# Kernel tuning notes

Measured on AMD Instinct MI355X. Metric: run time of the kernel, lower is better.

## Reference

```python
import jax, jax.numpy as jnp
import numpy as np

H = 8      # heads
S = 64     # size per head
EPS = 1e-5

def _ln(x, g, b):
    # LayerNorm over last axis with scale+offset (haiku hk.LayerNorm([-1], True, True))
    m = jnp.mean(x, axis=-1, keepdims=True)
    v = jnp.mean(jnp.square(x - m), axis=-1, keepdims=True)
    return (x - m) * jax.lax.rsqrt(v + EPS) * g + b

def setup_inputs() -> dict:
    key = jax.random.key(0)
    ks = jax.random.split(key, 10)
    N, C, K, CP = 16384, 512, 32, 128
    local = jax.random.normal(ks[0], (N, C), dtype=jnp.float32)
    pair = jax.random.normal(ks[1], (N, K, CP), dtype=jnp.float32)
    neighbours = jax.random.randint(ks[2], (N, K), 0, N, dtype=jnp.int64)
    mask = jnp.ones((N, K), dtype=bool)
    # parameters
    w_qkv = jax.random.normal(ks[3], (C, H * 3 * S), dtype=jnp.float32) / np.sqrt(C)
    g_q = jnp.ones((S,), jnp.float32); b_q = jnp.zeros((S,), jnp.float32)
    g_k = jnp.ones((S,), jnp.float32); b_k = jnp.zeros((S,), jnp.float32)
    w_bias = jax.random.normal(ks[4], (CP, H), dtype=jnp.float32) / np.sqrt(CP)
    d_cat = H * CP + H * S
    w_out = jax.random.normal(ks[5], (d_cat, C), dtype=jnp.float32) / np.sqrt(d_cat)
    b_out = jnp.zeros((C,), jnp.float32)
    return {"local": local, "pair": pair, "neighbours": neighbours, "mask": mask,
            "w_qkv": w_qkv, "g_q": g_q, "b_q": b_q, "g_k": g_k, "b_k": b_k,
            "w_bias": w_bias, "w_out": w_out, "b_out": b_out}

def reference(local, pair, neighbours, mask, w_qkv, g_q, b_q, g_k, b_k, w_bias, w_out, b_out):
    N = local.shape[0]
    qkv = (local @ w_qkv).reshape(N, H, 3 * S)          # [N, H, 3S]
    q, k, v = jnp.split(qkv, 3, axis=-1)                # each [N, H, S]
    q = _ln(q, g_q, b_q)
    k = _ln(k, g_k, b_k)
    bias = jnp.einsum('ijc,ch->ijh', pair, w_bias)      # [N, K, H]
    k_n = k[neighbours]                                 # [N, K, H, S]
    v_n = v[neighbours]                                 # [N, K, H, S]
    dot = jnp.einsum('ihc,ijhc->ijh', q, k_n) * (1.0 / np.sqrt(S))
    w_L = np.sqrt(0.5).astype(np.float32)
    logits = w_L * (dot + bias)                         # [N, K, H]
    pair_mask = mask & (neighbours != -1)               # [N, K]
    logits = jnp.where(pair_mask[..., None], logits, -1e9)
    attn = jax.nn.softmax(logits, axis=-2)              # softmax over neighbours K
    attn = jnp.where(pair_mask[..., None], attn, 0.0)
    out_pair = jnp.einsum('ijh,ijc->ihc', attn, pair)   # [N, H, CP]
    out_scalar = jnp.einsum('ijh,ijhc->ihc', attn, v_n) # [N, H, S]
    cat = jnp.concatenate((out_pair.reshape(N, -1), out_scalar.reshape(N, -1)), axis=-1)
    out = cat @ w_out + b_out                           # [N, C]
    return out.astype(local.dtype)
```

## Files before the change

kernel.cpp:

```cpp
#include <hip/hip_runtime.h>
#include <hip/hip_bf16.h>
#include <cstdint>

#define NTOK 16384
#define CDIM 512
#define KNB 32
#define CPD 128
#define NH 8
#define SD 64
#define QKV_W 1536
#define DCAT 1536

typedef __attribute__((ext_vector_type(8))) short short8;
typedef __attribute__((ext_vector_type(4))) float f32x4;

__device__ inline float bl16(unsigned w) { return __uint_as_float(w << 16); }
__device__ inline float bh16(unsigned w) { return __uint_as_float(w & 0xffff0000u); }

__device__ inline ushort bf2u(float x) {
    __hip_bfloat16 b = __float2bfloat16(x);
    return *(const ushort*)&b;
}

__device__ inline void gload_lds16(const void* g, void* l) {
    __builtin_amdgcn_global_load_lds((const __attribute__((address_space(1))) void*)g,
                                     (__attribute__((address_space(3))) void*)l, 16, 0, 0);
}

__global__ __launch_bounds__(256) void cvt_bf16_kernel(const float4* __restrict__ in,
                                                       ushort4* __restrict__ out, int n4)
{
    const int idx = blockIdx.x * 256 + threadIdx.x;
    if (idx < n4) {
        const float4 v = in[idx];
        ushort4 o;
        o.x = bf2u(v.x); o.y = bf2u(v.y); o.z = bf2u(v.z); o.w = bf2u(v.w);
        out[idx] = o;
    }
}

__global__ __launch_bounds__(256) void transpose_cvt(const float* __restrict__ in,
                                                     __hip_bfloat16* __restrict__ out,
                                                     int R, int Cc)
{
    __shared__ float t[32][33];
    const int c0 = blockIdx.x * 32, r0 = blockIdx.y * 32;
    const int tx = threadIdx.x & 31, ty = threadIdx.x >> 5;
    #pragma unroll
    for (int rr = ty; rr < 32; rr += 8)
        t[rr][tx] = in[(size_t)(r0 + rr) * Cc + c0 + tx];
    __syncthreads();
    #pragma unroll
    for (int rr = ty; rr < 32; rr += 8)
        out[(size_t)(c0 + rr) * R + r0 + tx] = __float2bfloat16(t[tx][rr]);
}

template<bool ADD_BIAS>
__global__ __launch_bounds__(256) void gemm_bf16(const ushort* __restrict__ A,
                                                 const ushort* __restrict__ Bt,
                                                 const float* __restrict__ bias,
                                                 float* __restrict__ C,
                                                 int M, int N, int K)
{
    __shared__ __align__(16) ushort Asl[128 * 32];
    __shared__ __align__(16) ushort Bsl[128 * 32];

    const int tid = threadIdx.x;
    const int wave = tid >> 6;
    const int lane = tid & 63;
    const int m0 = blockIdx.y * 128;
    const int n0 = blockIdx.x * 128;
    const int wr = wave >> 1, wc = wave & 1;

    f32x4 acc[4][4] = {};

    const int st_row_in_chunk = lane >> 2;
    const int st_bcol = (lane & 3) * 16;

    const int lr = lane & 15;
    const int kg = lane >> 4;

    for (int kt = 0; kt < K; kt += 32) {
        #pragma unroll
        for (int p = 0; p < 2; ++p) {
            const int chunk = wave * 2 + p;
            const int row = chunk * 16 + st_row_in_chunk;
            const char* asrc = (const char*)(A + (size_t)(m0 + row) * K + kt) + st_bcol;
            const char* bsrc = (const char*)(Bt + (size_t)(n0 + row) * K + kt) + st_bcol;
            gload_lds16(asrc, (char*)Asl + chunk * 1024);
            gload_lds16(bsrc, (char*)Bsl + chunk * 1024);
        }
        __syncthreads();

        short8 a[4], b[4];
        #pragma unroll
        for (int m = 0; m < 4; ++m)
            a[m] = *(const short8*)&Asl[(wr * 64 + m * 16 + lr) * 32 + kg * 8];
        #pragma unroll
        for (int n = 0; n < 4; ++n)
            b[n] = *(const short8*)&Bsl[(wc * 64 + n * 16 + lr) * 32 + kg * 8];
        #pragma unroll
        for (int m = 0; m < 4; ++m)
            #pragma unroll
            for (int n = 0; n < 4; ++n)
                acc[m][n] = __builtin_amdgcn_mfma_f32_16x16x32_bf16(a[m], b[n], acc[m][n], 0, 0, 0);
        __syncthreads();
    }

    #pragma unroll
    for (int m = 0; m < 4; ++m) {
        #pragma unroll
        for (int n = 0; n < 4; ++n) {
            const int col = n0 + wc * 64 + n * 16 + lr;
            const float bv = ADD_BIAS ? bias[col] : 0.0f;
            #pragma unroll
            for (int r = 0; r < 4; ++r) {
                const int row = m0 + wr * 64 + m * 16 + kg * 4 + r;
                C[(size_t)row * N + col] = acc[m][n][r] + bv;
            }
        }
    }
}

__global__ __launch_bounds__(256) void ln_kernel(const float* __restrict__ qkv,
                                                 const float* __restrict__ g_q,
                                                 const float* __restrict__ b_q,
                                                 const float* __restrict__ g_k,
                                                 const float* __restrict__ b_k,
                                                 __hip_bfloat16* __restrict__ qc,
                                                 __hip_bfloat16* __restrict__ kc,
                                                 __hip_bfloat16* __restrict__ vc)
{
    const int gid = blockIdx.x * 4 + (threadIdx.x >> 6);
    const int lane = threadIdx.x & 63;

    const float* p = qkv + (size_t)(gid >> 3) * QKV_W + (gid & 7) * 192;
    const float q = p[lane];
    const float k = p[64 + lane];
    const float v = p[128 + lane];

    float sq = q, sk = k;
    #pragma unroll
    for (int o = 1; o < 64; o <<= 1) { sq += __shfl_xor(sq, o); sk += __shfl_xor(sk, o); }
    const float mq = sq * (1.0f / 64.0f), mk = sk * (1.0f / 64.0f);
    const float dq = q - mq, dk = k - mk;
    float vq = dq * dq, vk = dk * dk;
    #pragma unroll
    for (int o = 1; o < 64; o <<= 1) { vq += __shfl_xor(vq, o); vk += __shfl_xor(vk, o); }
    const float iq = rsqrtf(vq * (1.0f / 64.0f) + 1e-5f);
    const float ik = rsqrtf(vk * (1.0f / 64.0f) + 1e-5f);

    const size_t o64 = (size_t)gid * 64 + lane;
    qc[o64] = __float2bfloat16(dq * iq * g_q[lane] + b_q[lane]);
    kc[o64] = __float2bfloat16(dk * ik * g_k[lane] + b_k[lane]);
    vc[o64] = __float2bfloat16(v);
}

__global__ __launch_bounds__(256) void attn_kernel(const __hip_bfloat16* __restrict__ qc,
                                                   const __hip_bfloat16* __restrict__ kc,
                                                   const __hip_bfloat16* __restrict__ vc,
                                                   const float* __restrict__ pair,
                                                   const int* __restrict__ nbr,
                                                   const float* __restrict__ w_bias,
                                                   __hip_bfloat16* __restrict__ cat)
{
    __shared__ __align__(16) ushort s_pairb[KNB][CPD + 8];
    __shared__ __align__(16) ushort s_wbTb[NH][CPD + 8];
    __shared__ __align__(16) ushort s_qb[NH][SD + 8];
    __shared__ __align__(16) float s_att[NH][KNB + 4];
    __shared__ __align__(16) float s_att2[NH][KNB + 4];
    __shared__ int s_nb[KNB];

    const int i = blockIdx.x;
    const int tid = threadIdx.x;
    const int j = tid >> 3;
    const int h = tid & 7;
    const int wave = tid >> 6;
    const int lane = tid & 63;

    const int rowj = nbr[i * KNB + j];
    const int rk = rowj < 0 ? 0 : rowj;
    const uint4* kp = (const uint4*)(kc + ((size_t)rk * NH + h) * SD);
    uint4 ka0 = kp[0], ka1 = kp[1], ka2 = kp[2], ka3 = kp[3];

    if (tid < KNB) s_nb[tid] = nbr[i * KNB + tid];
    if (tid < 64) {
        const uint4 qw = ((const uint4*)(qc + (size_t)i * 512))[tid];
        *(uint4*)&s_qb[tid >> 3][(tid & 7) * 8] = qw;
    }
    {
        const float4 w4 = ((const float4*)w_bias)[tid];
        const int c = tid >> 1;
        const int h0 = (tid & 1) * 4;
        s_wbTb[h0 + 0][c] = bf2u(w4.x);
        s_wbTb[h0 + 1][c] = bf2u(w4.y);
        s_wbTb[h0 + 2][c] = bf2u(w4.z);
        s_wbTb[h0 + 3][c] = bf2u(w4.w);
    }
    {
        const float4* pr = (const float4*)(pair + (size_t)i * KNB * CPD);
        #pragma unroll
        for (int t2 = 0; t2 < 2; ++t2) {
            const int ch = t2 * 256 + tid;
            const int row = ch >> 4;
            const int c8 = (ch & 15) * 8;
            const float4 a = pr[row * 32 + (c8 >> 2)];
            const float4 b = pr[row * 32 + (c8 >> 2) + 1];
            short8 o;
            o[0] = (short)bf2u(a.x); o[1] = (short)bf2u(a.y);
            o[2] = (short)bf2u(a.z); o[3] = (short)bf2u(a.w);
            o[4] = (short)bf2u(b.x); o[5] = (short)bf2u(b.y);
            o[6] = (short)bf2u(b.z); o[7] = (short)bf2u(b.w);
            *(short8*)&s_pairb[row][c8] = o;
        }
    }
    __syncthreads();

    uint4 kb0 = kp[4], kb1 = kp[5], kb2 = kp[6], kb3 = kp[7];

    const uint4* qrow = (const uint4*)&s_qb[h][0];
    float d0 = 0.f, d1 = 0.f, d2 = 0.f, d3 = 0.f;
    #pragma unroll
    for (int u = 0; u < 4; ++u) {
        uint4 K;
        switch (u) { case 0: K = ka0; break; case 1: K = ka1; break;
                     case 2: K = ka2; break; default: K = ka3; break; }
        const uint4 Q = qrow[u];
        d0 = fmaf(bl16(K.x), bl16(Q.x), fmaf(bh16(K.x), bh16(Q.x), d0));
        d1 = fmaf(bl16(K.y), bl16(Q.y), fmaf(bh16(K.y), bh16(Q.y), d1));
        d2 = fmaf(bl16(K.z), bl16(Q.z), fmaf(bh16(K.z), bh16(Q.z), d2));
        d3 = fmaf(bl16(K.w), bl16(Q.w), fmaf(bh16(K.w), bh16(Q.w), d3));
    }

    if (wave < 2) {
        const int lr = lane & 15;
        const int kg = lane >> 4;
        f32x4 cacc = {};
        const ushort* arow = &s_pairb[wave * 16 + lr][kg * 8];
        const ushort* brow = &s_wbTb[lr & 7][kg * 8];
        #pragma unroll
        for (int ks = 0; ks < 4; ++ks) {
            const short8 af = *(const short8*)(arow + ks * 32);
            const short8 bf = *(const short8*)(brow + ks * 32);
            cacc = __builtin_amdgcn_mfma_f32_16x16x32_bf16(af, bf, cacc, 0, 0, 0);
        }
        if (lr < 8) {
            const int jj = wave * 16 + kg * 4;
            s_att[lr][jj + 0] = cacc[0];
            s_att[lr][jj + 1] = cacc[1];
            s_att[lr][jj + 2] = cacc[2];
            s_att[lr][jj + 3] = cacc[3];
        }
    }

    #pragma unroll
    for (int u = 0; u < 4; ++u) {
        uint4 K;
        switch (u) { case 0: K = kb0; break; case 1: K = kb1; break;
                     case 2: K = kb2; break; default: K = kb3; break; }
        const uint4 Q = qrow[u + 4];
        d0 = fmaf(bl16(K.x), bl16(Q.x), fmaf(bh16(K.x), bh16(Q.x), d0));
        d1 = fmaf(bl16(K.y), bl16(Q.y), fmaf(bh16(K.y), bh16(Q.y), d1));
        d2 = fmaf(bl16(K.z), bl16(Q.z), fmaf(bh16(K.z), bh16(Q.z), d2));
        d3 = fmaf(bl16(K.w), bl16(Q.w), fmaf(bh16(K.w), bh16(Q.w), d3));
    }
    __syncthreads();

    float logit = -1e9f;
    if (rowj >= 0) {
        const float dot = (d0 + d1) + (d2 + d3);
        logit = 0.70710678118f * (dot * 0.125f + s_att[h][j]);
    }
    s_att[h][j] = logit;
    __syncthreads();

    const int slot = wave * 16 + (lane & 15);
    const int jg = lane >> 4;
    const int hh = slot >> 3;
    const char* vbase = (const char*)vc;
    uint4 va0, va1, va2, va3;
    {
        const int r0 = s_nb[jg * 8 + 0] < 0 ? 0 : s_nb[jg * 8 + 0];
        const int r1 = s_nb[jg * 8 + 1] < 0 ? 0 : s_nb[jg * 8 + 1];
        const int r2 = s_nb[jg * 8 + 2] < 0 ? 0 : s_nb[jg * 8 + 2];
        const int r3 = s_nb[jg * 8 + 3] < 0 ? 0 : s_nb[jg * 8 + 3];
        va0 = *(const uint4*)(vbase + (size_t)r0 * 1024 + slot * 16);
        va1 = *(const uint4*)(vbase + (size_t)r1 * 1024 + slot * 16);
        va2 = *(const uint4*)(vbase + (size_t)r2 * 1024 + slot * 16);
        va3 = *(const uint4*)(vbase + (size_t)r3 * 1024 + slot * 16);
    }

    {
        float mx = -1e30f;
        #pragma unroll
        for (int t = 0; t < 8; ++t) {
            const float4 w = *(const float4*)&s_att[h][t * 4];
            mx = fmaxf(mx, fmaxf(fmaxf(w.x, w.y), fmaxf(w.z, w.w)));
        }
        float s0 = 0.f, s1 = 0.f;
        #pragma unroll
        for (int t = 0; t < 8; ++t) {
            const float4 w = *(const float4*)&s_att[h][t * 4];
            s0 += __expf(w.x - mx) + __expf(w.z - mx);
            s1 += __expf(w.y - mx) + __expf(w.w - mx);
        }
        float aval = __expf(logit - mx) / (s0 + s1);
        if (rowj < 0) aval = 0.0f;
        s_att2[h][j] = aval;
    }
    __syncthreads();

    const float4 w0 = *(const float4*)&s_att2[hh][jg * 8];
    const float4 w1 = *(const float4*)&s_att2[hh][jg * 8 + 4];

    float acc0 = 0.f, acc1 = 0.f, acc2 = 0.f, acc3 = 0.f;
    float acc4 = 0.f, acc5 = 0.f, acc6 = 0.f, acc7 = 0.f;
    {
        const float a0 = w0.x, a1 = w0.y, a2 = w0.z, a3 = w0.w;
        acc0 = fmaf(a0, bl16(va0.x), acc0); acc1 = fmaf(a0, bh16(va0.x), acc1);
        acc2 = fmaf(a0, bl16(va0.y), acc2); acc3 = fmaf(a0, bh16(va0.y), acc3);
        acc4 = fmaf(a0, bl16(va0.z), acc4); acc5 = fmaf(a0, bh16(va0.z), acc5);
        acc6 = fmaf(a0, bl16(va0.w), acc6); acc7 = fmaf(a0, bh16(va0.w), acc7);
        acc0 = fmaf(a1, bl16(va1.x), acc0); acc1 = fmaf(a1, bh16(va1.x), acc1);
        acc2 = fmaf(a1, bl16(va1.y), acc2); acc3 = fmaf(a1, bh16(va1.y), acc3);
        acc4 = fmaf(a1, bl16(va1.z), acc4); acc5 = fmaf(a1, bh16(va1.z), acc5);
        acc6 = fmaf(a1, bl16(va1.w), acc6); acc7 = fmaf(a1, bh16(va1.w), acc7);
        acc0 = fmaf(a2, bl16(va2.x), acc0); acc1 = fmaf(a2, bh16(va2.x), acc1);
        acc2 = fmaf(a2, bl16(va2.y), acc2); acc3 = fmaf(a2, bh16(va2.y), acc3);
        acc4 = fmaf(a2, bl16(va2.z), acc4); acc5 = fmaf(a2, bh16(va2.z), acc5);
        acc6 = fmaf(a2, bl16(va2.w), acc6); acc7 = fmaf(a2, bh16(va2.w), acc7);
        acc0 = fmaf(a3, bl16(va3.x), acc0); acc1 = fmaf(a3, bh16(va3.x), acc1);
        acc2 = fmaf(a3, bl16(va3.y), acc2); acc3 = fmaf(a3, bh16(va3.y), acc3);
        acc4 = fmaf(a3, bl16(va3.z), acc4); acc5 = fmaf(a3, bh16(va3.z), acc5);
        acc6 = fmaf(a3, bl16(va3.w), acc6); acc7 = fmaf(a3, bh16(va3.w), acc7);
    }
    asm volatile("" ::: "memory");
    uint4 vb0, vb1, vb2, vb3;
    {
        const int r4 = s_nb[jg * 8 + 4] < 0 ? 0 : s_nb[jg * 8 + 4];
        const int r5 = s_nb[jg * 8 + 5] < 0 ? 0 : s_nb[jg * 8 + 5];
        const int r6 = s_nb[jg * 8 + 6] < 0 ? 0 : s_nb[jg * 8 + 6];
        const int r7 = s_nb[jg * 8 + 7] < 0 ? 0 : s_nb[jg * 8 + 7];
        vb0 = *(const uint4*)(vbase + (size_t)r4 * 1024 + slot * 16);
        vb1 = *(const uint4*)(vbase + (size_t)r5 * 1024 + slot * 16);
        vb2 = *(const uint4*)(vbase + (size_t)r6 * 1024 + slot * 16);
        vb3 = *(const uint4*)(vbase + (size_t)r7 * 1024 + slot * 16);
    }
    asm volatile("" ::: "memory");

    {
        const int h2 = tid >> 5;
        const int c0 = (tid & 31) * 4;
        float4 aA = make_float4(0.f, 0.f, 0.f, 0.f);
        float4 aB = make_float4(0.f, 0.f, 0.f, 0.f);
        #pragma unroll
        for (int t = 0; t < 8; ++t) {
            const float4 aw = *(const float4*)&s_att2[h2][t * 4];
            const uint2 p0 = *(const uint2*)&s_pairb[t * 4 + 0][c0];
            const uint2 p1 = *(const uint2*)&s_pairb[t * 4 + 1][c0];
            const uint2 p2 = *(const uint2*)&s_pairb[t * 4 + 2][c0];
            const uint2 p3 = *(const uint2*)&s_pairb[t * 4 + 3][c0];
            aA.x = fmaf(aw.x, bl16(p0.x), aA.x); aA.y = fmaf(aw.x, bh16(p0.x), aA.y);
            aA.z = fmaf(aw.x, bl16(p0.y), aA.z); aA.w = fmaf(aw.x, bh16(p0.y), aA.w);
            aB.x = fmaf(aw.y, bl16(p1.x), aB.x); aB.y = fmaf(aw.y, bh16(p1.x), aB.y);
            aB.z = fmaf(aw.y, bl16(p1.y), aB.z); aB.w = fmaf(aw.y, bh16(p1.y), aB.w);
            aA.x = fmaf(aw.z, bl16(p2.x), aA.x); aA.y = fmaf(aw.z, bh16(p2.x), aA.y);
            aA.z = fmaf(aw.z, bl16(p2.y), aA.z); aA.w = fmaf(aw.z, bh16(p2.y), aA.w);
            aB.x = fmaf(aw.w, bl16(p3.x), aB.x); aB.y = fmaf(aw.w, bh16(p3.x), aB.y);
            aB.z = fmaf(aw.w, bl16(p3.y), aB.z); aB.w = fmaf(aw.w, bh16(p3.y), aB.w);
        }
        ushort4 o;
        o.x = bf2u(aA.x + aB.x); o.y = bf2u(aA.y + aB.y);
        o.z = bf2u(aA.z + aB.z); o.w = bf2u(aA.w + aB.w);
        *(ushort4*)&cat[(size_t)i * DCAT + h2 * CPD + c0] = o;
    }

    {
        const float a4 = w1.x, a5 = w1.y, a6 = w1.z, a7 = w1.w;
        acc0 = fmaf(a4, bl16(vb0.x), acc0); acc1 = fmaf(a4, bh16(vb0.x), acc1);
        acc2 = fmaf(a4, bl16(vb0.y), acc2); acc3 = fmaf(a4, bh16(vb0.y), acc3);
        acc4 = fmaf(a4, bl16(vb0.z), acc4); acc5 = fmaf(a4, bh16(vb0.z), acc5);
        acc6 = fmaf(a4, bl16(vb0.w), acc6); acc7 = fmaf(a4, bh16(vb0.w), acc7);
        acc0 = fmaf(a5, bl16(vb1.x), acc0); acc1 = fmaf(a5, bh16(vb1.x), acc1);
        acc2 = fmaf(a5, bl16(vb1.y), acc2); acc3 = fmaf(a5, bh16(vb1.y), acc3);
        acc4 = fmaf(a5, bl16(vb1.z), acc4); acc5 = fmaf(a5, bh16(vb1.z), acc5);
        acc6 = fmaf(a5, bl16(vb1.w), acc6); acc7 = fmaf(a5, bh16(vb1.w), acc7);
        acc0 = fmaf(a6, bl16(vb2.x), acc0); acc1 = fmaf(a6, bh16(vb2.x), acc1);
        acc2 = fmaf(a6, bl16(vb2.y), acc2); acc3 = fmaf(a6, bh16(vb2.y), acc3);
        acc4 = fmaf(a6, bl16(vb2.z), acc4); acc5 = fmaf(a6, bh16(vb2.z), acc5);
        acc6 = fmaf(a6, bl16(vb2.w), acc6); acc7 = fmaf(a6, bh16(vb2.w), acc7);
        acc0 = fmaf(a7, bl16(vb3.x), acc0); acc1 = fmaf(a7, bh16(vb3.x), acc1);
        acc2 = fmaf(a7, bl16(vb3.y), acc2); acc3 = fmaf(a7, bh16(vb3.y), acc3);
        acc4 = fmaf(a7, bl16(vb3.z), acc4); acc5 = fmaf(a7, bh16(vb3.z), acc5);
        acc6 = fmaf(a7, bl16(vb3.w), acc6); acc7 = fmaf(a7, bh16(vb3.w), acc7);
    }
    acc0 += __shfl_xor(acc0, 16); acc0 += __shfl_xor(acc0, 32);
    acc1 += __shfl_xor(acc1, 16); acc1 += __shfl_xor(acc1, 32);
    acc2 += __shfl_xor(acc2, 16); acc2 += __shfl_xor(acc2, 32);
    acc3 += __shfl_xor(acc3, 16); acc3 += __shfl_xor(acc3, 32);
    acc4 += __shfl_xor(acc4, 16); acc4 += __shfl_xor(acc4, 32);
    acc5 += __shfl_xor(acc5, 16); acc5 += __shfl_xor(acc5, 32);
    acc6 += __shfl_xor(acc6, 16); acc6 += __shfl_xor(acc6, 32);
    acc7 += __shfl_xor(acc7, 16); acc7 += __shfl_xor(acc7, 32);
    if (jg == 0) {
        short8 o;
        o[0] = (short)bf2u(acc0); o[1] = (short)bf2u(acc1);
        o[2] = (short)bf2u(acc2); o[3] = (short)bf2u(acc3);
        o[4] = (short)bf2u(acc4); o[5] = (short)bf2u(acc5);
        o[6] = (short)bf2u(acc6); o[7] = (short)bf2u(acc7);
        char* dst = (char*)cat + ((size_t)i * DCAT + NH * CPD) * 2 + slot * 16;
        *(short8*)dst = o;
    }
}

extern "C" void kernel_launch(void* const* d_in, const int* in_sizes, int n_in,
                              void* d_out, int out_size, void* d_ws, size_t ws_size,
                              hipStream_t stream)
{
    const float* local  = (const float*)d_in[0];
    const float* pair   = (const float*)d_in[1];
    const int*   nbr    = (const int*)d_in[2];
    const float* w_qkv  = (const float*)d_in[4];
    const float* g_q    = (const float*)d_in[5];
    const float* b_q    = (const float*)d_in[6];
    const float* g_k    = (const float*)d_in[7];
    const float* b_k    = (const float*)d_in[8];
    const float* w_bias = (const float*)d_in[9];
    const float* w_out  = (const float*)d_in[10];
    const float* b_out  = (const float*)d_in[11];
    float* out = (float*)d_out;

    char* base = (char*)d_ws;
    float*          qkv   = (float*)base;
    __hip_bfloat16* cat_b = (__hip_bfloat16*)base;
    ushort*         lc    = (ushort*)(base + 100663296u);
    __hip_bfloat16* wqkvT = (__hip_bfloat16*)(base + 117440512u);
    __hip_bfloat16* woutT = (__hip_bfloat16*)(base + 119013376u);
    __hip_bfloat16* qc    = (__hip_bfloat16*)(base + 120586240u);
    __hip_bfloat16* kc    = (__hip_bfloat16*)(base + 137363456u);
    __hip_bfloat16* vc    = (__hip_bfloat16*)(base + 154140672u);

    cvt_bf16_kernel<<<(NTOK * CDIM / 4 + 255) / 256, 256, 0, stream>>>(
        (const float4*)local, (ushort4*)lc, NTOK * CDIM / 4);
    transpose_cvt<<<dim3(QKV_W / 32, CDIM / 32), 256, 0, stream>>>(w_qkv, wqkvT, CDIM, QKV_W);
    transpose_cvt<<<dim3(CDIM / 32, DCAT / 32), 256, 0, stream>>>(w_out, woutT, DCAT, CDIM);

    hipLaunchKernelGGL((gemm_bf16<false>), dim3(QKV_W / 128, NTOK / 128), dim3(256), 0, stream,
                       lc, (const ushort*)wqkvT, nullptr, qkv, NTOK, QKV_W, CDIM);

    ln_kernel<<<NTOK * NH / 4, 256, 0, stream>>>(qkv, g_q, b_q, g_k, b_k, qc, kc, vc);

    attn_kernel<<<NTOK, 256, 0, stream>>>(qc, kc, vc, pair, nbr, w_bias, cat_b);

    hipLaunchKernelGGL((gemm_bf16<true>), dim3(CDIM / 128, NTOK / 128), dim3(256), 0, stream,
                       (const ushort*)cat_b, (const ushort*)woutT, b_out, out, NTOK, CDIM, DCAT);
}
```

Baseline: 358.2 us.

## Store QKV projection as bf16 and software-pipeline gathered K/V loads

The QKV GEMM now writes bf16 instead of fp32, which halves the intermediate write and the later read by the layer-norm kernel. The layer-norm kernel reads bf16 and passes V through unchanged. In the attention kernel, the gathered K and V row loads are restructured into a two-register rotating pipeline with compiler barriers, interleaving loads with the FMAs to cut register pressure while keeping loads in flight. Rounding q/k to bf16 before layer norm adds a small precision loss.

```diff
diff --git a/kernel.cpp b/kernel.cpp
--- a/kernel.cpp
+++ b/kernel.cpp
@@ -16,6 +16,7 @@
 
 __device__ inline float bl16(unsigned w) { return __uint_as_float(w << 16); }
 __device__ inline float bh16(unsigned w) { return __uint_as_float(w & 0xffff0000u); }
+__device__ inline float u16f(ushort u) { return __uint_as_float(((unsigned)u) << 16); }
 
 __device__ inline ushort bf2u(float x) {
     __hip_bfloat16 b = __float2bfloat16(x);
@@ -55,11 +56,11 @@
         out[(size_t)(c0 + rr) * R + r0 + tx] = __float2bfloat16(t[tx][rr]);
 }
 
-template<bool ADD_BIAS>
+template<bool ADD_BIAS, bool OUT_BF16>
 __global__ __launch_bounds__(256) void gemm_bf16(const ushort* __restrict__ A,
                                                  const ushort* __restrict__ Bt,
                                                  const float* __restrict__ bias,
-                                                 float* __restrict__ C,
+                                                 void* __restrict__ Cv,
                                                  int M, int N, int K)
 {
     __shared__ __align__(16) ushort Asl[128 * 32];
@@ -116,13 +117,16 @@
             #pragma unroll
             for (int r = 0; r < 4; ++r) {
                 const int row = m0 + wr * 64 + m * 16 + kg * 4 + r;
-                C[(size_t)row * N + col] = acc[m][n][r] + bv;
+                if (OUT_BF16)
+                    ((ushort*)Cv)[(size_t)row * N + col] = bf2u(acc[m][n][r] + bv);
+                else
+                    ((float*)Cv)[(size_t)row * N + col] = acc[m][n][r] + bv;
             }
         }
     }
 }
 
-__global__ __launch_bounds__(256) void ln_kernel(const float* __restrict__ qkv,
+__global__ __launch_bounds__(256) void ln_kernel(const ushort* __restrict__ qkvb,
                                                  const float* __restrict__ g_q,
                                                  const float* __restrict__ b_q,
                                                  const float* __restrict__ g_k,
@@ -134,10 +138,10 @@
     const int gid = blockIdx.x * 4 + (threadIdx.x >> 6);
     const int lane = threadIdx.x & 63;
 
-    const float* p = qkv + (size_t)(gid >> 3) * QKV_W + (gid & 7) * 192;
-    const float q = p[lane];
-    const float k = p[64 + lane];
-    const float v = p[128 + lane];
+    const ushort* p = qkvb + (size_t)(gid >> 3) * QKV_W + (gid & 7) * 192;
+    const float q = u16f(p[lane]);
+    const float k = u16f(p[64 + lane]);
+    const ushort v = p[128 + lane];
 
     float sq = q, sk = k;
     #pragma unroll
@@ -153,7 +157,7 @@
     const size_t o64 = (size_t)gid * 64 + lane;
     qc[o64] = __float2bfloat16(dq * iq * g_q[lane] + b_q[lane]);
     kc[o64] = __float2bfloat16(dk * ik * g_k[lane] + b_k[lane]);
-    vc[o64] = __float2bfloat16(v);
+    *(ushort*)&vc[o64] = v;
 }
 
 __global__ __launch_bounds__(256) void attn_kernel(const __hip_bfloat16* __restrict__ qc,
@@ -181,7 +185,7 @@
     const int rowj = nbr[i * KNB + j];
     const int rk = rowj < 0 ? 0 : rowj;
     const uint4* kp = (const uint4*)(kc + ((size_t)rk * NH + h) * SD);
-    uint4 ka0 = kp[0], ka1 = kp[1], ka2 = kp[2], ka3 = kp[3];
+    uint4 kA0 = kp[0], kA1 = kp[1];
 
     if (tid < KNB) s_nb[tid] = nbr[i * KNB + tid];
     if (tid < 64) {
@@ -216,21 +220,22 @@
     }
     __syncthreads();
 
-    uint4 kb0 = kp[4], kb1 = kp[5], kb2 = kp[6], kb3 = kp[7];
-
     const uint4* qrow = (const uint4*)&s_qb[h][0];
     float d0 = 0.f, d1 = 0.f, d2 = 0.f, d3 = 0.f;
-    #pragma unroll
-    for (int u = 0; u < 4; ++u) {
-        uint4 K;
-        switch (u) { case 0: K = ka0; break; case 1: K = ka1; break;
-                     case 2: K = ka2; break; default: K = ka3; break; }
-        const uint4 Q = qrow[u];
-        d0 = fmaf(bl16(K.x), bl16(Q.x), fmaf(bh16(K.x), bh16(Q.x), d0));
-        d1 = fmaf(bl16(K.y), bl16(Q.y), fmaf(bh16(K.y), bh16(Q.y), d1));
-        d2 = fmaf(bl16(K.z), bl16(Q.z), fmaf(bh16(K.z), bh16(Q.z), d2));
-        d3 = fmaf(bl16(K.w), bl16(Q.w), fmaf(bh16(K.w), bh16(Q.w), d3));
-    }
+
+#define DOT_CHUNK(KV, u) do { \
+        const uint4 Q = qrow[u]; \
+        d0 = fmaf(bl16(KV.x), bl16(Q.x), fmaf(bh16(KV.x), bh16(Q.x), d0)); \
+        d1 = fmaf(bl16(KV.y), bl16(Q.y), fmaf(bh16(KV.y), bh16(Q.y), d1)); \
+        d2 = fmaf(bl16(KV.z), bl16(Q.z), fmaf(bh16(KV.z), bh16(Q.z), d2)); \
+        d3 = fmaf(bl16(KV.w), bl16(Q.w), fmaf(bh16(KV.w), bh16(Q.w), d3)); \
+    } while (0)
+
+    uint4 kB0 = kp[2], kB1 = kp[3];
+    asm volatile("" ::: "memory");
+    DOT_CHUNK(kA0, 0); DOT_CHUNK(kA1, 1);
+    kA0 = kp[4]; kA1 = kp[5];
+    asm volatile("" ::: "memory");
 
     if (wave < 2) {
         const int lr = lane & 15;
@@ -253,17 +258,12 @@
         }
     }
 
-    #pragma unroll
-    for (int u = 0; u < 4; ++u) {
-        uint4 K;
-        switch (u) { case 0: K = kb0; break; case 1: K = kb1; break;
-                     case 2: K = kb2; break; default: K = kb3; break; }
-        const uint4 Q = qrow[u + 4];
-        d0 = fmaf(bl16(K.x), bl16(Q.x), fmaf(bh16(K.x), bh16(Q.x), d0));
-        d1 = fmaf(bl16(K.y), bl16(Q.y), fmaf(bh16(K.y), bh16(Q.y), d1));
-        d2 = fmaf(bl16(K.z), bl16(Q.z), fmaf(bh16(K.z), bh16(Q.z), d2));
-        d3 = fmaf(bl16(K.w), bl16(Q.w), fmaf(bh16(K.w), bh16(Q.w), d3));
-    }
+    DOT_CHUNK(kB0, 2); DOT_CHUNK(kB1, 3);
+    kB0 = kp[6]; kB1 = kp[7];
+    asm volatile("" ::: "memory");
+    DOT_CHUNK(kA0, 4); DOT_CHUNK(kA1, 5);
+    DOT_CHUNK(kB0, 6); DOT_CHUNK(kB1, 7);
+#undef DOT_CHUNK
     __syncthreads();
 
     float logit = -1e9f;
@@ -278,17 +278,17 @@
     const int jg = lane >> 4;
     const int hh = slot >> 3;
     const char* vbase = (const char*)vc;
-    uint4 va0, va1, va2, va3;
-    {
-        const int r0 = s_nb[jg * 8 + 0] < 0 ? 0 : s_nb[jg * 8 + 0];
-        const int r1 = s_nb[jg * 8 + 1] < 0 ? 0 : s_nb[jg * 8 + 1];
-        const int r2 = s_nb[jg * 8 + 2] < 0 ? 0 : s_nb[jg * 8 + 2];
-        const int r3 = s_nb[jg * 8 + 3] < 0 ? 0 : s_nb[jg * 8 + 3];
-        va0 = *(const uint4*)(vbase + (size_t)r0 * 1024 + slot * 16);
-        va1 = *(const uint4*)(vbase + (size_t)r1 * 1024 + slot * 16);
-        va2 = *(const uint4*)(vbase + (size_t)r2 * 1024 + slot * 16);
-        va3 = *(const uint4*)(vbase + (size_t)r3 * 1024 + slot * 16);
-    }
+
+#define VLOAD(u) (*(const uint4*)(vbase + (size_t)(s_nb[jg * 8 + (u)] < 0 ? 0 : s_nb[jg * 8 + (u)]) * 1024 + slot * 16))
+#define VACC(V, a) do { \
+        acc0 = fmaf(a, bl16(V.x), acc0); acc1 = fmaf(a, bh16(V.x), acc1); \
+        acc2 = fmaf(a, bl16(V.y), acc2); acc3 = fmaf(a, bh16(V.y), acc3); \
+        acc4 = fmaf(a, bl16(V.z), acc4); acc5 = fmaf(a, bh16(V.z), acc5); \
+        acc6 = fmaf(a, bl16(V.w), acc6); acc7 = fmaf(a, bh16(V.w), acc7); \
+    } while (0)
+
+    uint4 vA0 = VLOAD(0), vA1 = VLOAD(1);
+    asm volatile("" ::: "memory");
 
     {
         float mx = -1e30f;
@@ -315,37 +315,14 @@
 
     float acc0 = 0.f, acc1 = 0.f, acc2 = 0.f, acc3 = 0.f;
     float acc4 = 0.f, acc5 = 0.f, acc6 = 0.f, acc7 = 0.f;
-    {
-        const float a0 = w0.x, a1 = w0.y, a2 = w0.z, a3 = w0.w;
-        acc0 = fmaf(a0, bl16(va0.x), acc0); acc1 = fmaf(a0, bh16(va0.x), acc1);
-        acc2 = fmaf(a0, bl16(va0.y), acc2); acc3 = fmaf(a0, bh16(va0.y), acc3);
-        acc4 = fmaf(a0, bl16(va0.z), acc4); acc5 = fmaf(a0, bh16(va0.z), acc5);
-        acc6 = fmaf(a0, bl16(va0.w), acc6); acc7 = fmaf(a0, bh16(va0.w), acc7);
-        acc0 = fmaf(a1, bl16(va1.x), acc0); acc1 = fmaf(a1, bh16(va1.x), acc1);
-        acc2 = fmaf(a1, bl16(va1.y), acc2); acc3 = fmaf(a1, bh16(va1.y), acc3);
-        acc4 = fmaf(a1, bl16(va1.z), acc4); acc5 = fmaf(a1, bh16(va1.z), acc5);
-        acc6 = fmaf(a1, bl16(va1.w), acc6); acc7 = fmaf(a1, bh16(va1.w), acc7);
-        acc0 = fmaf(a2, bl16(va2.x), acc0); acc1 = fmaf(a2, bh16(va2.x), acc1);
-        acc2 = fmaf(a2, bl16(va2.y), acc2); acc3 = fmaf(a2, bh16(va2.y), acc3);
-        acc4 = fmaf(a2, bl16(va2.z), acc4); acc5 = fmaf(a2, bh16(va2.z), acc5);
-        acc6 = fmaf(a2, bl16(va2.w), acc6); acc7 = fmaf(a2, bh16(va2.w), acc7);
-        acc0 = fmaf(a3, bl16(va3.x), acc0); acc1 = fmaf(a3, bh16(va3.x), acc1);
-        acc2 = fmaf(a3, bl16(va3.y), acc2); acc3 = fmaf(a3, bh16(va3.y), acc3);
-        acc4 = fmaf(a3, bl16(va3.z), acc4); acc5 = fmaf(a3, bh16(va3.z), acc5);
-        acc6 = fmaf(a3, bl16(va3.w), acc6); acc7 = fmaf(a3, bh16(va3.w), acc7);
-    }
-    asm volatile("" ::: "memory");
-    uint4 vb0, vb1, vb2, vb3;
-    {
-        const int r4 = s_nb[jg * 8 + 4] < 0 ? 0 : s_nb[jg * 8 + 4];
-        const int r5 = s_nb[jg * 8 + 5] < 0 ? 0 : s_nb[jg * 8 + 5];
-        const int r6 = s_nb[jg * 8 + 6] < 0 ? 0 : s_nb[jg * 8 + 6];
-        const int r7 = s_nb[jg * 8 + 7] < 0 ? 0 : s_nb[jg * 8 + 7];
-        vb0 = *(const uint4*)(vbase + (size_t)r4 * 1024 + slot * 16);
-        vb1 = *(const uint4*)(vbase + (size_t)r5 * 1024 + slot * 16);
-        vb2 = *(const uint4*)(vbase + (size_t)r6 * 1024 + slot * 16);
-        vb3 = *(const uint4*)(vbase + (size_t)r7 * 1024 + slot * 16);
-    }
+
+    uint4 vB0 = VLOAD(2), vB1 = VLOAD(3);
+    asm volatile("" ::: "memory");
+    VACC(vA0, w0.x); VACC(vA1, w0.y);
+    vA0 = VLOAD(4); vA1 = VLOAD(5);
+    asm volatile("" ::: "memory");
+    VACC(vB0, w0.z); VACC(vB1, w0.w);
+    vB0 = VLOAD(6); vB1 = VLOAD(7);
     asm volatile("" ::: "memory");
 
     {
@@ -375,25 +352,10 @@
         *(ushort4*)&cat[(size_t)i * DCAT + h2 * CPD + c0] = o;
     }
 
-    {
-        const float a4 = w1.x, a5 = w1.y, a6 = w1.z, a7 = w1.w;
-        acc0 = fmaf(a4, bl16(vb0.x), acc0); acc1 = fmaf(a4, bh16(vb0.x), acc1);
-        acc2 = fmaf(a4, bl16(vb0.y), acc2); acc3 = fmaf(a4, bh16(vb0.y), acc3);
-        acc4 = fmaf(a4, bl16(vb0.z), acc4); acc5 = fmaf(a4, bh16(vb0.z), acc5);
-        acc6 = fmaf(a4, bl16(vb0.w), acc6); acc7 = fmaf(a4, bh16(vb0.w), acc7);
-        acc0 = fmaf(a5, bl16(vb1.x), acc0); acc1 = fmaf(a5, bh16(vb1.x), acc1);
-        acc2 = fmaf(a5, bl16(vb1.y), acc2); acc3 = fmaf(a5, bh16(vb1.y), acc3);
-        acc4 = fmaf(a5, bl16(vb1.z), acc4); acc5 = fmaf(a5, bh16(vb1.z), acc5);
-        acc6 = fmaf(a5, bl16(vb1.w), acc6); acc7 = fmaf(a5, bh16(vb1.w), acc7);
-        acc0 = fmaf(a6, bl16(vb2.x), acc0); acc1 = fmaf(a6, bh16(vb2.x), acc1);
-        acc2 = fmaf(a6, bl16(vb2.y), acc2); acc3 = fmaf(a6, bh16(vb2.y), acc3);
-        acc4 = fmaf(a6, bl16(vb2.z), acc4); acc5 = fmaf(a6, bh16(vb2.z), acc5);
-        acc6 = fmaf(a6, bl16(vb2.w), acc6); acc7 = fmaf(a6, bh16(vb2.w), acc7);
-        acc0 = fmaf(a7, bl16(vb3.x), acc0); acc1 = fmaf(a7, bh16(vb3.x), acc1);
-        acc2 = fmaf(a7, bl16(vb3.y), acc2); acc3 = fmaf(a7, bh16(vb3.y), acc3);
-        acc4 = fmaf(a7, bl16(vb3.z), acc4); acc5 = fmaf(a7, bh16(vb3.z), acc5);
-        acc6 = fmaf(a7, bl16(vb3.w), acc6); acc7 = fmaf(a7, bh16(vb3.w), acc7);
-    }
+    VACC(vA0, w1.x); VACC(vA1, w1.y);
+    VACC(vB0, w1.z); VACC(vB1, w1.w);
+#undef VLOAD
+#undef VACC
     acc0 += __shfl_xor(acc0, 16); acc0 += __shfl_xor(acc0, 32);
     acc1 += __shfl_xor(acc1, 16); acc1 += __shfl_xor(acc1, 32);
     acc2 += __shfl_xor(acc2, 16); acc2 += __shfl_xor(acc2, 32);
@@ -431,7 +393,7 @@
     float* out = (float*)d_out;
 
     char* base = (char*)d_ws;
-    float*          qkv   = (float*)base;
+    ushort*         qkvb  = (ushort*)base;
     __hip_bfloat16* cat_b = (__hip_bfloat16*)base;
     ushort*         lc    = (ushort*)(base + 100663296u);
     __hip_bfloat16* wqkvT = (__hip_bfloat16*)(base + 117440512u);
@@ -445,13 +407,13 @@
     transpose_cvt<<<dim3(QKV_W / 32, CDIM / 32), 256, 0, stream>>>(w_qkv, wqkvT, CDIM, QKV_W);
     transpose_cvt<<<dim3(CDIM / 32, DCAT / 32), 256, 0, stream>>>(w_out, woutT, DCAT, CDIM);
 
-    hipLaunchKernelGGL((gemm_bf16<false>), dim3(QKV_W / 128, NTOK / 128), dim3(256), 0, stream,
-                       lc, (const ushort*)wqkvT, nullptr, qkv, NTOK, QKV_W, CDIM);
-
-    ln_kernel<<<NTOK * NH / 4, 256, 0, stream>>>(qkv, g_q, b_q, g_k, b_k, qc, kc, vc);
+    hipLaunchKernelGGL((gemm_bf16<false, true>), dim3(QKV_W / 128, NTOK / 128), dim3(256), 0, stream,
+                       lc, (const ushort*)wqkvT, nullptr, (void*)qkvb, NTOK, QKV_W, CDIM);
+
+    ln_kernel<<<NTOK * NH / 4, 256, 0, stream>>>(qkvb, g_q, b_q, g_k, b_k, qc, kc, vc);
 
     attn_kernel<<<NTOK, 256, 0, stream>>>(qc, kc, vc, pair, nbr, w_bias, cat_b);
 
-    hipLaunchKernelGGL((gemm_bf16<true>), dim3(CDIM / 128, NTOK / 128), dim3(256), 0, stream,
-                       (const ushort*)cat_b, (const ushort*)woutT, b_out, out, NTOK, CDIM, DCAT);
-}
+    hipLaunchKernelGGL((gemm_bf16<true, false>), dim3(CDIM / 128, NTOK / 128), dim3(256), 0, stream,
+                       (const ushort*)cat_b, (const ushort*)woutT, b_out, (void*)out, NTOK, CDIM, DCAT);
+}
```

Measured after the change: 352.4 us. About the same (-1.6%).
